# Optimization experiments

Hardware: AMD Instinct MI355X
Metric: run time of the kernel (lower is better)

Reference implementation:

```python
import jax, jax.numpy as jnp
import numpy as np

DIM = 384
HEADS = 12
WS = 7
HID = 4 * 256  # FFN hidden is hard-coded default 1024, NOT 4*dim
EPS = 1e-5


def layernorm(x, g, b):
    mu = jnp.mean(x, axis=-1, keepdims=True)
    var = jnp.mean(jnp.square(x - mu), axis=-1, keepdims=True)
    return (x - mu) * jax.lax.rsqrt(var + EPS) * g + b


def setup_inputs() -> dict:
    key = jax.random.key(0)
    ks = jax.random.split(key, 12)
    s = 0.02
    return {
        "x": jax.random.normal(ks[0], (32, DIM, 56, 56), dtype=jnp.float32),
        "ln1_g": jnp.ones((DIM,), jnp.float32),
        "ln1_b": jnp.zeros((DIM,), jnp.float32),
        "qkv_w": jax.random.normal(ks[1], (3 * DIM, DIM), jnp.float32) * s,
        "qkv_b": jnp.zeros((3 * DIM,), jnp.float32),
        "proj_w": jax.random.normal(ks[2], (DIM, DIM), jnp.float32) * s,
        "proj_b": jnp.zeros((DIM,), jnp.float32),
        "ln2_g": jnp.ones((DIM,), jnp.float32),
        "ln2_b": jnp.zeros((DIM,), jnp.float32),
        "fc1_w": jax.random.normal(ks[3], (HID, DIM), jnp.float32) * s,
        "fc1_b": jnp.zeros((HID,), jnp.float32),
        "fc2_w": jax.random.normal(ks[4], (DIM, HID), jnp.float32) * s,
        "fc2_b": jnp.zeros((DIM,), jnp.float32),
    }


def window_attention(x, qkv_w, qkv_b, proj_w, proj_b):
    # x: [B, H, W, C] channels-last
    B, H, W, C = x.shape
    Wh, Ww = H // WS, W // WS
    # partition: [B*Wh*Ww, WS*WS, C]
    w = x.reshape(B, Wh, WS, Ww, WS, C).transpose(0, 1, 3, 2, 4, 5)
    w = w.reshape(B * Wh * Ww, WS * WS, C)
    Bn, N, _ = w.shape
    hd = C // HEADS
    qkv = w @ qkv_w.T + qkv_b  # [Bn, N, 3C]
    qkv = qkv.reshape(Bn, N, 3, HEADS, hd).transpose(2, 0, 3, 1, 4)
    q, k, v = qkv[0], qkv[1], qkv[2]  # each [Bn, h, N, hd]
    attn = jnp.einsum('bhnd,bhmd->bhnm', q, k) * (hd ** -0.5)
    attn = jax.nn.softmax(attn, axis=-1)
    o = jnp.einsum('bhnm,bhmd->bhnd', attn, v)
    o = o.transpose(0, 2, 1, 3).reshape(Bn, N, C)
    o = o @ proj_w.T + proj_b
    # reverse
    o = o.reshape(B, Wh, Ww, WS, WS, C).transpose(0, 1, 3, 2, 4, 5)
    return o.reshape(B, H, W, C)


def reference(x, ln1_g, ln1_b, qkv_w, qkv_b, proj_w, proj_b,
              ln2_g, ln2_b, fc1_w, fc1_b, fc2_w, fc2_b):
    # x: [B, C, H, W]
    residual = x
    h = x.transpose(0, 2, 3, 1)  # [B,H,W,C]
    h = layernorm(h, ln1_g, ln1_b)
    h = window_attention(h, qkv_w, qkv_b, proj_w, proj_b)
    x = h.transpose(0, 3, 1, 2) + residual
    residual = x
    h = x.transpose(0, 2, 3, 1)
    h = layernorm(h, ln2_g, ln2_b)
    h = jax.nn.gelu(h @ fc1_w.T + fc1_b, approximate=False)
    h = h @ fc2_w.T + fc2_b
    return h.transpose(0, 3, 1, 2) + residual
```

## Files before the change

kernel.cpp:

```cpp
#include <hip/hip_runtime.h>
#include <cstdint>
#include <cmath>

#define DIM 384
#define HEADS 12
#define TOKENS 100352
#define HW_ 3136
#define NWIN 2048

typedef __attribute__((ext_vector_type(8))) short short8;
typedef __attribute__((ext_vector_type(4))) short short4v;
typedef __attribute__((ext_vector_type(2))) short short2v;
typedef __attribute__((ext_vector_type(4))) float f32x4;

#define AS1 __attribute__((address_space(1)))
#define AS3 __attribute__((address_space(3)))

__device__ __forceinline__ short f2b(float f){
  unsigned u = __builtin_bit_cast(unsigned, f);
  u += 0x7FFFu + ((u >> 16) & 1u);
  return (short)(u >> 16);
}
__device__ __forceinline__ float b2f(short h){
  unsigned u = ((unsigned)(unsigned short)h) << 16;
  return __builtin_bit_cast(float, u);
}

__device__ __forceinline__ void gload_lds16(const short* g, short* l){
  __builtin_amdgcn_global_load_lds((AS1 void*)(g), (AS3 void*)(l), 16, 0, 0);
}

__global__ void k_cvt(const float* __restrict__ s, short* __restrict__ d, int n){
  int i = blockIdx.x*256 + threadIdx.x;
  if (i < n) d[i] = f2b(s[i]);
}

__global__ __launch_bounds__(256) void k_ln1(const float* __restrict__ x,
    const float* __restrict__ gam, const float* __restrict__ bet,
    short* __restrict__ ln1, short* __restrict__ xr)
{
  __shared__ float red0[256];
  __shared__ float red1[256];
  __shared__ float mus[64], rss[64];
  __shared__ short lnc[64*36];
  __shared__ short xc[64*36];
  int t = threadIdx.x;
  int blk = blockIdx.x;
  int b = blk / 49;
  int hw0 = (blk % 49) * 64;
  int p = t & 63, cq = t >> 6;
  const float* xb = x + (long)b*DIM*HW_ + hw0 + p;
  float s = 0.f, sq = 0.f;
  for (int i = 0; i < 96; i++){
    int c = i*4 + cq;
    float v = xb[(long)c*HW_];
    s += v; sq += v*v;
  }
  red0[t] = s; red1[t] = sq;
  __syncthreads();
  if (t < 64){
    float ts = red0[t] + red0[t+64] + red0[t+128] + red0[t+192];
    float tq = red1[t] + red1[t+64] + red1[t+128] + red1[t+192];
    float mu = ts * (1.f/DIM);
    float var = tq * (1.f/DIM) - mu*mu;
    mus[t] = mu;
    rss[t] = rsqrtf(var + 1e-5f);
  }
  __syncthreads();
  float mu_p = mus[p], rs_p = rss[p];
  int p2 = t >> 2, q4 = t & 3;
  int hwp2 = hw0 + p2;
  int h2 = hwp2 / 56, w2 = hwp2 % 56;
  int wt2 = ((b*8 + h2/7)*8 + w2/7)*49 + (h2%7)*7 + (w2%7);
  long lnbase = (long)wt2*DIM;
  long xrbase = (long)(b*HW_ + hwp2)*DIM;
  for (int cc0 = 0; cc0 < DIM; cc0 += 32){
    #pragma unroll
    for (int u = 0; u < 8; u++){
      int c = cc0 + cq*8 + u;
      float v = xb[(long)c*HW_];
      float nv = (v - mu_p)*rs_p*gam[c] + bet[c];
      lnc[p*36 + cq*8 + u] = f2b(nv);
      xc[p*36 + cq*8 + u] = f2b(v);
    }
    __syncthreads();
    short8 av, bv;
    #pragma unroll
    for (int u = 0; u < 8; u++){
      av[u] = lnc[p2*36 + q4*8 + u];
      bv[u] = xc[p2*36 + q4*8 + u];
    }
    *(short8*)(ln1 + lnbase + cc0 + q4*8) = av;
    *(short8*)(xr + xrbase + cc0 + q4*8) = bv;
    __syncthreads();
  }
}

#define EPI_BIAS 0
#define EPI_PROJ 1
#define EPI_GELU 2
#define EPI_RES  3

template<int EPI>
__global__ __launch_bounds__(256) void k_gemm(
    const short* __restrict__ A, const short* __restrict__ B,
    const float* __restrict__ bias, short* __restrict__ out,
    const short* __restrict__ res, int M, int N, int K, int ntiles)
{
  __shared__ float smemf[8448];
  short* AsP = (short*)smemf;
  short* BsP = (short*)(smemf + 4096);
  float* E   = smemf;

  int nwg = gridDim.x;
  int orig = blockIdx.x;
  int bid = (orig & 7) * (nwg >> 3) + (orig >> 3);
  int nt = bid % ntiles, mt = bid / ntiles;
  int m0 = mt*128, n0 = nt*128;
  int t = threadIdx.x;
  int lane = t & 63, wv = t >> 6;
  int wm = wv >> 1, wn = wv & 1;
  int gg = lane >> 4, cc = lane & 15;

  int srow = t >> 2;
  int skc = ((t & 3) ^ (srow & 3)) << 3;
  const short* Ab = A + (long)(m0 + srow)*K + skc;
  const short* Bb = B + (long)(n0 + srow)*K + skc;
  long rowstep = 64L*K;

  int goff = (gg << 3) ^ ((cc & 3) << 3);

  f32x4 acc[4][4];
  #pragma unroll
  for (int i=0;i<4;i++)
    #pragma unroll
    for (int j=0;j<4;j++) acc[i][j] = (f32x4){0.f,0.f,0.f,0.f};

  gload_lds16(Ab,           AsP + t*8);
  gload_lds16(Ab + rowstep, AsP + (t+256)*8);
  gload_lds16(Bb,           BsP + t*8);
  gload_lds16(Bb + rowstep, BsP + (t+256)*8);

  int nk = K >> 5;
  for (int kt = 0; kt < nk; kt++){
    int cur = kt & 1;
    __syncthreads();
    if (kt + 1 < nk){
      int nxt = cur ^ 1;
      long ko = (long)(kt + 1) << 5;
      gload_lds16(Ab + ko,           AsP + nxt*4096 + t*8);
      gload_lds16(Ab + ko + rowstep, AsP + nxt*4096 + (t+256)*8);
      gload_lds16(Bb + ko,           BsP + nxt*4096 + t*8);
      gload_lds16(Bb + ko + rowstep, BsP + nxt*4096 + (t+256)*8);
    }
    const short* Ac = AsP + cur*4096;
    const short* Bc = BsP + cur*4096;
    short8 af[4], bfv[4];
    #pragma unroll
    for (int mi=0;mi<4;mi++) af[mi] = *(const short8*)(Ac + (wm*64 + mi*16 + cc)*32 + goff);
    #pragma unroll
    for (int ni=0;ni<4;ni++) bfv[ni] = *(const short8*)(Bc + (wn*64 + ni*16 + cc)*32 + goff);
    #pragma unroll
    for (int mi=0;mi<4;mi++)
      #pragma unroll
      for (int ni=0;ni<4;ni++)
        acc[mi][ni] = __builtin_amdgcn_mfma_f32_16x16x32_bf16(af[mi], bfv[ni], acc[mi][ni], 0, 0, 0);
  }

  #pragma unroll
  for (int p = 0; p < 2; p++){
    __syncthreads();
    #pragma unroll
    for (int mh = 0; mh < 2; mh++){
      #pragma unroll
      for (int r = 0; r < 4; r++){
        int crow = wm*32 + mh*16 + gg*4 + r;
        float* Er = E + crow*132 + wn*64 + cc;
        Er[0]  = acc[mh*2 + p][0][r];
        Er[16] = acc[mh*2 + p][1][r];
        Er[32] = acc[mh*2 + p][2][r];
        Er[48] = acc[mh*2 + p][3][r];
      }
    }
    __syncthreads();
    #pragma unroll
    for (int jj = 0; jj < 8; jj++){
      int unit = jj*256 + t;
      int crow = unit >> 5, chunk = unit & 31;
      int rr = crow & 15, mh = (crow >> 4) & 1, wmr = crow >> 5;
      int row = m0 + wmr*64 + (mh*2 + p)*16 + rr;
      int col = n0 + chunk*4;
      f32x4 v = *(const f32x4*)(E + crow*132 + chunk*4);
      f32x4 bv = *(const f32x4*)(bias + col);
      long orow;
      if constexpr (EPI == EPI_PROJ) {
        int b = row / HW_; int rem = row % HW_;
        int wid = rem / 49, idx = rem % 49;
        int hh = (wid >> 3)*7 + idx/7;
        int ww = (wid & 7)*7 + idx%7;
        orow = (long)(b*HW_ + hh*56 + ww)*N;
      } else {
        orow = (long)row*N;
      }
      float vv[4];
      #pragma unroll
      for (int j = 0; j < 4; j++){
        vv[j] = v[j] + bv[j];
        if constexpr (EPI == EPI_GELU)
          vv[j] = 0.5f*vv[j]*(1.f + erff(vv[j]*0.70710678118654752f));
      }
      if constexpr (EPI == EPI_PROJ || EPI == EPI_RES){
        short4v rv = *(const short4v*)(res + orow + col);
        #pragma unroll
        for (int j = 0; j < 4; j++) vv[j] += b2f(rv[j]);
      }
      short4v ov;
      #pragma unroll
      for (int j = 0; j < 4; j++) ov[j] = f2b(vv[j]);
      *(short4v*)(out + orow + col) = ov;
    }
  }
}

__global__ __launch_bounds__(256) void k_attn(const short* __restrict__ qkv, short* __restrict__ o)
{
  __shared__ short lds[4*7424];
  int t = threadIdx.x;
  int lane = t & 63, wv = t >> 6;
  int w = blockIdx.x;
  short* Qs = lds + wv*7424;
  short* Ks = Qs + 2560;
  short* Vt = Ks + 2560;
  short* Pl = Qs;
  int g = lane >> 4, c = lane & 15;
  int nrow = lane >> 2;
  int dc = (lane & 3) * 8;
  const float scale = 0.17677669529663687f;
  for (int hh = 0; hh < 3; hh++){
    int h = wv + hh*4;
    __syncthreads();
    long base = (long)w*49*1152 + h*32;
    #pragma unroll
    for (int it = 0; it < 4; it++){
      int n = it*16 + nrow;
      short8 vq = {0,0,0,0,0,0,0,0};
      short8 vk = vq, vvv = vq;
      if (n < 49){
        vq  = *(const short8*)(qkv + base + (long)n*1152 + dc);
        vk  = *(const short8*)(qkv + base + (long)n*1152 + 384 + dc);
        vvv = *(const short8*)(qkv + base + (long)n*1152 + 768 + dc);
      }
      *(short8*)(Qs + n*40 + dc) = vq;
      *(short8*)(Ks + n*40 + dc) = vk;
      #pragma unroll
      for (int u = 0; u < 8; u++) Vt[(dc+u)*72 + n] = vvv[u];
    }
    __syncthreads();
    f32x4 sacc[4][4];
    #pragma unroll
    for (int i=0;i<4;i++)
      #pragma unroll
      for (int j=0;j<4;j++) sacc[i][j] = (f32x4){0.f,0.f,0.f,0.f};
    short8 kf[4];
    #pragma unroll
    for (int ni=0;ni<4;ni++) kf[ni] = *(const short8*)(Ks + (ni*16 + c)*40 + g*8);
    #pragma unroll
    for (int mi=0;mi<4;mi++){
      short8 a = *(const short8*)(Qs + (mi*16 + c)*40 + g*8);
      #pragma unroll
      for (int ni=0;ni<4;ni++)
        sacc[mi][ni] = __builtin_amdgcn_mfma_f32_16x16x32_bf16(a, kf[ni], sacc[mi][ni], 0, 0, 0);
    }
    #pragma unroll
    for (int mi=0;mi<4;mi++){
      #pragma unroll
      for (int r=0;r<4;r++){
        float v0 = sacc[mi][0][r]*scale;
        float v1 = sacc[mi][1][r]*scale;
        float v2 = sacc[mi][2][r]*scale;
        float v3 = (c >= 1) ? -1e30f : sacc[mi][3][r]*scale;
        float mx = fmaxf(fmaxf(v0,v1), fmaxf(v2,v3));
        #pragma unroll
        for (int off=1; off<16; off<<=1) mx = fmaxf(mx, __shfl_xor(mx, off));
        float e0 = __expf(v0-mx), e1 = __expf(v1-mx), e2 = __expf(v2-mx), e3 = __expf(v3-mx);
        float sm = e0+e1+e2+e3;
        #pragma unroll
        for (int off=1; off<16; off<<=1) sm += __shfl_xor(sm, off);
        float inv = 1.f/sm;
        int prow = mi*16 + g*4 + r;
        Pl[prow*72 +      c] = f2b(e0*inv);
        Pl[prow*72 + 16 + c] = f2b(e1*inv);
        Pl[prow*72 + 32 + c] = f2b(e2*inv);
        Pl[prow*72 + 48 + c] = f2b(e3*inv);
      }
    }
    __syncthreads();
    f32x4 oacc[4][2];
    #pragma unroll
    for (int i=0;i<4;i++){ oacc[i][0] = (f32x4){0.f,0.f,0.f,0.f}; oacc[i][1] = oacc[i][0]; }
    #pragma unroll
    for (int ks=0; ks<2; ks++){
      short8 bb0 = *(const short8*)(Vt + (c)*72      + ks*32 + g*8);
      short8 bb1 = *(const short8*)(Vt + (16 + c)*72 + ks*32 + g*8);
      #pragma unroll
      for (int mi=0;mi<4;mi++){
        short8 aa = *(const short8*)(Pl + (mi*16 + c)*72 + ks*32 + g*8);
        oacc[mi][0] = __builtin_amdgcn_mfma_f32_16x16x32_bf16(aa, bb0, oacc[mi][0], 0, 0, 0);
        oacc[mi][1] = __builtin_amdgcn_mfma_f32_16x16x32_bf16(aa, bb1, oacc[mi][1], 0, 0, 0);
      }
    }
    #pragma unroll
    for (int mi=0;mi<4;mi++){
      #pragma unroll
      for (int r=0;r<4;r++){
        int row = mi*16 + g*4 + r;
        if (row < 49){
          long ob = ((long)w*49 + row)*384 + h*32;
          o[ob + c]      = f2b(oacc[mi][0][r]);
          o[ob + 16 + c] = f2b(oacc[mi][1][r]);
        }
      }
    }
  }
}

__global__ __launch_bounds__(256) void k_ln2(const short* __restrict__ x2,
  const float* __restrict__ gam, const float* __restrict__ bet, short* __restrict__ o)
{
  int t = threadIdx.x, lane = t & 63, wv = t >> 6;
  long row = (long)blockIdx.x*4 + wv;
  const short* xr = x2 + row*DIM;
  short4v a = *(const short4v*)(xr + lane*4);
  short2v b2 = *(const short2v*)(xr + 256 + lane*2);
  float f[6] = {b2f(a[0]),b2f(a[1]),b2f(a[2]),b2f(a[3]),b2f(b2[0]),b2f(b2[1])};
  float s = 0.f, sq = 0.f;
  #pragma unroll
  for (int i=0;i<6;i++){ s += f[i]; sq += f[i]*f[i]; }
  #pragma unroll
  for (int off=1; off<64; off<<=1){ s += __shfl_xor(s, off); sq += __shfl_xor(sq, off); }
  float mu = s*(1.f/DIM);
  float var = sq*(1.f/DIM) - mu*mu;
  float rs = rsqrtf(var + 1e-5f);
  int c0 = lane*4, c1 = 256 + lane*2;
  short4v oa; short2v ob;
  #pragma unroll
  for (int i=0;i<4;i++) oa[i] = f2b((f[i]-mu)*rs*gam[c0+i] + bet[c0+i]);
  #pragma unroll
  for (int j=0;j<2;j++) ob[j] = f2b((f[4+j]-mu)*rs*gam[c1+j] + bet[c1+j]);
  *(short4v*)(o + row*DIM + c0) = oa;
  *(short2v*)(o + row*DIM + c1) = ob;
}

__global__ __launch_bounds__(256) void k_out(const short* __restrict__ s, float* __restrict__ o)
{
  __shared__ short tile[64*392];
  int t = threadIdx.x;
  long tok0 = (long)blockIdx.x*64;
  int b = (int)(tok0 / HW_), hw0 = (int)(tok0 % HW_);
  #pragma unroll
  for (int i=0;i<12;i++){
    int unit = i*256 + t;
    int tok = unit / 48, slot = unit % 48;
    short8 v = *(const short8*)(s + (tok0+tok)*DIM + slot*8);
    int slotS = slot ^ (tok & 3);
    *(short8*)(tile + tok*392 + slotS*8) = v;
  }
  __syncthreads();
  int p = t & 63;
  int cq = t >> 6;
  for (int j=0;j<96;j++){
    int c = j*4 + cq;
    int sw = (c >> 3) ^ (p & 3);
    o[((long)b*DIM + c)*HW_ + hw0 + p] = b2f(tile[p*392 + sw*8 + (c & 7)]);
  }
}

extern "C" void kernel_launch(void* const* d_in, const int* in_sizes, int n_in,
                              void* d_out, int out_size, void* d_ws, size_t ws_size,
                              hipStream_t stream) {
  (void)in_sizes; (void)n_in; (void)out_size; (void)ws_size;
  const float* x      = (const float*)d_in[0];
  const float* ln1_g  = (const float*)d_in[1];
  const float* ln1_b  = (const float*)d_in[2];
  const float* qkv_w  = (const float*)d_in[3];
  const float* qkv_b  = (const float*)d_in[4];
  const float* proj_w = (const float*)d_in[5];
  const float* proj_b = (const float*)d_in[6];
  const float* ln2_g  = (const float*)d_in[7];
  const float* ln2_b  = (const float*)d_in[8];
  const float* fc1_w  = (const float*)d_in[9];
  const float* fc1_b  = (const float*)d_in[10];
  const float* fc2_w  = (const float*)d_in[11];
  const float* fc2_b  = (const float*)d_in[12];

  char* ws = (char*)d_ws;
  short* buf1 = (short*)(ws);
  short* buf2 = (short*)(ws + 231211008L);
  short* buf3 = (short*)(ws + 308281344L);
  short* buf4 = (short*)(ws + 385351680L);
  short* buf5 = (short*)(ws + 462422016L);
  short* wq = (short*)(ws + 539492352L);
  short* wp = wq + 442368;
  short* w1 = wp + 147456;
  short* w2 = w1 + 393216;

  k_cvt<<<dim3((442368+255)/256), dim3(256), 0, stream>>>(qkv_w, wq, 442368);
  k_cvt<<<dim3((147456+255)/256), dim3(256), 0, stream>>>(proj_w, wp, 147456);
  k_cvt<<<dim3((393216+255)/256), dim3(256), 0, stream>>>(fc1_w, w1, 393216);
  k_cvt<<<dim3((393216+255)/256), dim3(256), 0, stream>>>(fc2_w, w2, 393216);

  k_ln1<<<dim3(1568), dim3(256), 0, stream>>>(x, ln1_g, ln1_b, buf2, buf5);

  k_gemm<EPI_BIAS><<<dim3(784*9), dim3(256), 0, stream>>>(buf2, wq, qkv_b, buf1, nullptr,
                                                          TOKENS, 1152, 384, 9);
  k_attn<<<dim3(NWIN), dim3(256), 0, stream>>>(buf1, buf3);

  k_gemm<EPI_PROJ><<<dim3(784*3), dim3(256), 0, stream>>>(buf3, wp, proj_b, buf4, buf5,
                                                          TOKENS, 384, 384, 3);
  k_ln2<<<dim3(TOKENS/4), dim3(256), 0, stream>>>(buf4, ln2_g, ln2_b, buf2);

  k_gemm<EPI_GELU><<<dim3(784*8), dim3(256), 0, stream>>>(buf2, w1, fc1_b, buf1, nullptr,
                                                          TOKENS, 1024, 384, 8);
  k_gemm<EPI_RES><<<dim3(784*3), dim3(256), 0, stream>>>(buf1, w2, fc2_b, buf3, buf4,
                                                         TOKENS, 384, 1024, 3);
  k_out<<<dim3(1568), dim3(256), 0, stream>>>(buf3, (float*)d_out);
}
```

Baseline: 795.8 us.

## Fuse NCHW fp32 output transpose into fc2 GEMM epilogue; use fast GELU approximation

The fc2 GEMM epilogue now adds bias and residual, stages the tile in shared memory with a padded stride, and writes fp32 directly in channel-major NCHW layout. This removes the separate k_out transpose kernel and the bf16 round-trip of the final result. Separately, erff-based GELU is replaced by the Abramowitz-Stegun polynomial with rcp and exp, cutting the epilogue cost of the fc1 GEMM at a small accuracy cost. The attention kernel is only moved in the file.

```diff
diff --git a/kernel.cpp b/kernel.cpp
--- a/kernel.cpp
+++ b/kernel.cpp
@@ -28,6 +28,17 @@
 
 __device__ __forceinline__ void gload_lds16(const short* g, short* l){
   __builtin_amdgcn_global_load_lds((AS1 void*)(g), (AS3 void*)(l), 16, 0, 0);
+}
+
+__device__ __forceinline__ float gelu_f(float v){
+  float z  = v * 0.70710678118654752f;
+  float az = fabsf(z);
+  float t  = __builtin_amdgcn_rcpf(1.f + 0.3275911f*az);
+  float poly = t*(0.254829592f + t*(-0.284496736f + t*(1.421413741f +
+               t*(-1.453152027f + t*1.061405429f))));
+  float e  = __expf(-z*z);
+  float er = copysignf(1.f - poly*e, z);
+  return 0.5f * v * (1.f + er);
 }
 
 __global__ void k_cvt(const float* __restrict__ s, short* __restrict__ d, int n){
@@ -99,7 +110,7 @@
 #define EPI_BIAS 0
 #define EPI_PROJ 1
 #define EPI_GELU 2
-#define EPI_RES  3
+#define EPI_OUT  4
 
 template<int EPI>
 __global__ __launch_bounds__(256) void k_gemm(
@@ -107,7 +118,9 @@
     const float* __restrict__ bias, short* __restrict__ out,
     const short* __restrict__ res, int M, int N, int K, int ntiles)
 {
-  __shared__ float smemf[8448];
+  constexpr int ES  = (EPI == EPI_OUT) ? 133  : 132;
+  constexpr int SMF = (EPI == EPI_OUT) ? 8512 : 8448;
+  __shared__ float smemf[SMF];
   short* AsP = (short*)smemf;
   short* BsP = (short*)(smemf + 4096);
   float* E   = smemf;
@@ -167,158 +180,99 @@
         acc[mi][ni] = __builtin_amdgcn_mfma_f32_16x16x32_bf16(af[mi], bfv[ni], acc[mi][ni], 0, 0, 0);
   }
 
-  #pragma unroll
-  for (int p = 0; p < 2; p++){
-    __syncthreads();
-    #pragma unroll
-    for (int mh = 0; mh < 2; mh++){
-      #pragma unroll
-      for (int r = 0; r < 4; r++){
-        int crow = wm*32 + mh*16 + gg*4 + r;
-        float* Er = E + crow*132 + wn*64 + cc;
-        Er[0]  = acc[mh*2 + p][0][r];
-        Er[16] = acc[mh*2 + p][1][r];
-        Er[32] = acc[mh*2 + p][2][r];
-        Er[48] = acc[mh*2 + p][3][r];
-      }
-    }
-    __syncthreads();
-    #pragma unroll
-    for (int jj = 0; jj < 8; jj++){
-      int unit = jj*256 + t;
-      int crow = unit >> 5, chunk = unit & 31;
-      int rr = crow & 15, mh = (crow >> 4) & 1, wmr = crow >> 5;
-      int row = m0 + wmr*64 + (mh*2 + p)*16 + rr;
-      int col = n0 + chunk*4;
-      f32x4 v = *(const f32x4*)(E + crow*132 + chunk*4);
-      f32x4 bv = *(const f32x4*)(bias + col);
-      long orow;
-      if constexpr (EPI == EPI_PROJ) {
-        int b = row / HW_; int rem = row % HW_;
-        int wid = rem / 49, idx = rem % 49;
-        int hh = (wid >> 3)*7 + idx/7;
-        int ww = (wid & 7)*7 + idx%7;
-        orow = (long)(b*HW_ + hh*56 + ww)*N;
-      } else {
-        orow = (long)row*N;
-      }
-      float vv[4];
-      #pragma unroll
-      for (int j = 0; j < 4; j++){
-        vv[j] = v[j] + bv[j];
-        if constexpr (EPI == EPI_GELU)
-          vv[j] = 0.5f*vv[j]*(1.f + erff(vv[j]*0.70710678118654752f));
-      }
-      if constexpr (EPI == EPI_PROJ || EPI == EPI_RES){
-        short4v rv = *(const short4v*)(res + orow + col);
-        #pragma unroll
-        for (int j = 0; j < 4; j++) vv[j] += b2f(rv[j]);
-      }
-      short4v ov;
-      #pragma unroll
-      for (int j = 0; j < 4; j++) ov[j] = f2b(vv[j]);
-      *(short4v*)(out + orow + col) = ov;
-    }
-  }
-}
-
-__global__ __launch_bounds__(256) void k_attn(const short* __restrict__ qkv, short* __restrict__ o)
-{
-  __shared__ short lds[4*7424];
-  int t = threadIdx.x;
-  int lane = t & 63, wv = t >> 6;
-  int w = blockIdx.x;
-  short* Qs = lds + wv*7424;
-  short* Ks = Qs + 2560;
-  short* Vt = Ks + 2560;
-  short* Pl = Qs;
-  int g = lane >> 4, c = lane & 15;
-  int nrow = lane >> 2;
-  int dc = (lane & 3) * 8;
-  const float scale = 0.17677669529663687f;
-  for (int hh = 0; hh < 3; hh++){
-    int h = wv + hh*4;
-    __syncthreads();
-    long base = (long)w*49*1152 + h*32;
-    #pragma unroll
-    for (int it = 0; it < 4; it++){
-      int n = it*16 + nrow;
-      short8 vq = {0,0,0,0,0,0,0,0};
-      short8 vk = vq, vvv = vq;
-      if (n < 49){
-        vq  = *(const short8*)(qkv + base + (long)n*1152 + dc);
-        vk  = *(const short8*)(qkv + base + (long)n*1152 + 384 + dc);
-        vvv = *(const short8*)(qkv + base + (long)n*1152 + 768 + dc);
-      }
-      *(short8*)(Qs + n*40 + dc) = vq;
-      *(short8*)(Ks + n*40 + dc) = vk;
-      #pragma unroll
-      for (int u = 0; u < 8; u++) Vt[(dc+u)*72 + n] = vvv[u];
-    }
-    __syncthreads();
-    f32x4 sacc[4][4];
-    #pragma unroll
-    for (int i=0;i<4;i++)
-      #pragma unroll
-      for (int j=0;j<4;j++) sacc[i][j] = (f32x4){0.f,0.f,0.f,0.f};
-    short8 kf[4];
-    #pragma unroll
-    for (int ni=0;ni<4;ni++) kf[ni] = *(const short8*)(Ks + (ni*16 + c)*40 + g*8);
-    #pragma unroll
-    for (int mi=0;mi<4;mi++){
-      short8 a = *(const short8*)(Qs + (mi*16 + c)*40 + g*8);
-      #pragma unroll
-      for (int ni=0;ni<4;ni++)
-        sacc[mi][ni] = __builtin_amdgcn_mfma_f32_16x16x32_bf16(a, kf[ni], sacc[mi][ni], 0, 0, 0);
-    }
-    #pragma unroll
-    for (int mi=0;mi<4;mi++){
-      #pragma unroll
-      for (int r=0;r<4;r++){
-        float v0 = sacc[mi][0][r]*scale;
-        float v1 = sacc[mi][1][r]*scale;
-        float v2 = sacc[mi][2][r]*scale;
-        float v3 = (c >= 1) ? -1e30f : sacc[mi][3][r]*scale;
-        float mx = fmaxf(fmaxf(v0,v1), fmaxf(v2,v3));
-        #pragma unroll
-        for (int off=1; off<16; off<<=1) mx = fmaxf(mx, __shfl_xor(mx, off));
-        float e0 = __expf(v0-mx), e1 = __expf(v1-mx), e2 = __expf(v2-mx), e3 = __expf(v3-mx);
-        float sm = e0+e1+e2+e3;
-        #pragma unroll
-        for (int off=1; off<16; off<<=1) sm += __shfl_xor(sm, off);
-        float inv = 1.f/sm;
-        int prow = mi*16 + g*4 + r;
-        Pl[prow*72 +      c] = f2b(e0*inv);
-        Pl[prow*72 + 16 + c] = f2b(e1*inv);
-        Pl[prow*72 + 32 + c] = f2b(e2*inv);
-        Pl[prow*72 + 48 + c] = f2b(e3*inv);
-      }
-    }
-    __syncthreads();
-    f32x4 oacc[4][2];
-    #pragma unroll
-    for (int i=0;i<4;i++){ oacc[i][0] = (f32x4){0.f,0.f,0.f,0.f}; oacc[i][1] = oacc[i][0]; }
-    #pragma unroll
-    for (int ks=0; ks<2; ks++){
-      short8 bb0 = *(const short8*)(Vt + (c)*72      + ks*32 + g*8);
-      short8 bb1 = *(const short8*)(Vt + (16 + c)*72 + ks*32 + g*8);
-      #pragma unroll
-      for (int mi=0;mi<4;mi++){
-        short8 aa = *(const short8*)(Pl + (mi*16 + c)*72 + ks*32 + g*8);
-        oacc[mi][0] = __builtin_amdgcn_mfma_f32_16x16x32_bf16(aa, bb0, oacc[mi][0], 0, 0, 0);
-        oacc[mi][1] = __builtin_amdgcn_mfma_f32_16x16x32_bf16(aa, bb1, oacc[mi][1], 0, 0, 0);
-      }
-    }
-    #pragma unroll
-    for (int mi=0;mi<4;mi++){
-      #pragma unroll
-      for (int r=0;r<4;r++){
-        int row = mi*16 + g*4 + r;
-        if (row < 49){
-          long ob = ((long)w*49 + row)*384 + h*32;
-          o[ob + c]      = f2b(oacc[mi][0][r]);
-          o[ob + 16 + c] = f2b(oacc[mi][1][r]);
-        }
+  if constexpr (EPI == EPI_OUT) {
+    float* outf = (float*)out;
+    #pragma unroll
+    for (int p = 0; p < 2; p++){
+      __syncthreads();
+      if (wm == p){
+        #pragma unroll
+        for (int mi=0;mi<4;mi++){
+          #pragma unroll
+          for (int r=0;r<4;r++){
+            float* Er = E + (mi*16 + gg*4 + r)*ES + wn*64 + cc;
+            Er[0]  = acc[mi][0][r];
+            Er[16] = acc[mi][1][r];
+            Er[32] = acc[mi][2][r];
+            Er[48] = acc[mi][3][r];
+          }
+        }
+      }
+      __syncthreads();
+      #pragma unroll
+      for (int jj = 0; jj < 8; jj++){
+        int unit = jj*256 + t;
+        int crow = unit >> 5, chunk = unit & 31;
+        int row = m0 + p*64 + crow;
+        f32x4 v = *(const f32x4*)(E + crow*ES + chunk*4);
+        f32x4 bv = *(const f32x4*)(bias + n0 + chunk*4);
+        short4v rv = *(const short4v*)(res + (long)row*N + n0 + chunk*4);
+        #pragma unroll
+        for (int j = 0; j < 4; j++) v[j] += bv[j] + b2f(rv[j]);
+        *(f32x4*)(E + crow*ES + chunk*4) = v;
+      }
+      __syncthreads();
+      #pragma unroll
+      for (int jj = 0; jj < 32; jj++){
+        int unit = jj*256 + t;
+        int c = unit >> 6, rl = unit & 63;
+        int token = m0 + p*64 + rl;
+        int b = token / HW_;
+        int hw = token - b*HW_;
+        outf[((long)b*DIM + n0 + c)*HW_ + hw] = E[rl*ES + c];
+      }
+    }
+  } else {
+    #pragma unroll
+    for (int p = 0; p < 2; p++){
+      __syncthreads();
+      #pragma unroll
+      for (int mh = 0; mh < 2; mh++){
+        #pragma unroll
+        for (int r = 0; r < 4; r++){
+          int crow = wm*32 + mh*16 + gg*4 + r;
+          float* Er = E + crow*ES + wn*64 + cc;
+          Er[0]  = acc[mh*2 + p][0][r];
+          Er[16] = acc[mh*2 + p][1][r];
+          Er[32] = acc[mh*2 + p][2][r];
+          Er[48] = acc[mh*2 + p][3][r];
+        }
+      }
+      __syncthreads();
+      #pragma unroll
+      for (int jj = 0; jj < 8; jj++){
+        int unit = jj*256 + t;
+        int crow = unit >> 5, chunk = unit & 31;
+        int rr = crow & 15, mh = (crow >> 4) & 1, wmr = crow >> 5;
+        int row = m0 + wmr*64 + (mh*2 + p)*16 + rr;
+        int col = n0 + chunk*4;
+        f32x4 v = *(const f32x4*)(E + crow*ES + chunk*4);
+        f32x4 bv = *(const f32x4*)(bias + col);
+        long orow;
+        if constexpr (EPI == EPI_PROJ) {
+          int b = row / HW_; int rem = row % HW_;
+          int wid = rem / 49, idx = rem % 49;
+          int hh = (wid >> 3)*7 + idx/7;
+          int ww = (wid & 7)*7 + idx%7;
+          orow = (long)(b*HW_ + hh*56 + ww)*N;
+        } else {
+          orow = (long)row*N;
+        }
+        float vv[4];
+        #pragma unroll
+        for (int j = 0; j < 4; j++){
+          vv[j] = v[j] + bv[j];
+          if constexpr (EPI == EPI_GELU) vv[j] = gelu_f(vv[j]);
+        }
+        if constexpr (EPI == EPI_PROJ){
+          short4v rv = *(const short4v*)(res + orow + col);
+          #pragma unroll
+          for (int j = 0; j < 4; j++) vv[j] += b2f(rv[j]);
+        }
+        short4v ov;
+        #pragma unroll
+        for (int j = 0; j < 4; j++) ov[j] = f2b(vv[j]);
+        *(short4v*)(out + orow + col) = ov;
       }
     }
   }
@@ -351,27 +305,105 @@
   *(short2v*)(o + row*DIM + c1) = ob;
 }
 
-__global__ __launch_bounds__(256) void k_out(const short* __restrict__ s, float* __restrict__ o)
+__global__ __launch_bounds__(256) void k_attn(const short* __restrict__ qkv, short* __restrict__ o)
 {
-  __shared__ short tile[64*392];
+  __shared__ short lds[4*7424];
   int t = threadIdx.x;
-  long tok0 = (long)blockIdx.x*64;
-  int b = (int)(tok0 / HW_), hw0 = (int)(tok0 % HW_);
-  #pragma unroll
-  for (int i=0;i<12;i++){
-    int unit = i*256 + t;
-    int tok = unit / 48, slot = unit % 48;
-    short8 v = *(const short8*)(s + (tok0+tok)*DIM + slot*8);
-    int slotS = slot ^ (tok & 3);
-    *(short8*)(tile + tok*392 + slotS*8) = v;
-  }
-  __syncthreads();
-  int p = t & 63;
-  int cq = t >> 6;
-  for (int j=0;j<96;j++){
-    int c = j*4 + cq;
-    int sw = (c >> 3) ^ (p & 3);
-    o[((long)b*DIM + c)*HW_ + hw0 + p] = b2f(tile[p*392 + sw*8 + (c & 7)]);
+  int lane = t & 63, wv = t >> 6;
+  int w = blockIdx.x;
+  short* Qs = lds + wv*7424;
+  short* Ks = Qs + 2560;
+  short* Vt = Ks + 2560;
+  short* Pl = Qs;
+  int g = lane >> 4, c = lane & 15;
+  int nrow = lane >> 2;
+  int dc = (lane & 3) * 8;
+  const float scale = 0.17677669529663687f;
+  for (int hh = 0; hh < 3; hh++){
+    int h = wv + hh*4;
+    __syncthreads();
+    long base = (long)w*49*1152 + h*32;
+    #pragma unroll
+    for (int it = 0; it < 4; it++){
+      int n = it*16 + nrow;
+      short8 vq = {0,0,0,0,0,0,0,0};
+      short8 vk = vq, vvv = vq;
+      if (n < 49){
+        vq  = *(const short8*)(qkv + base + (long)n*1152 + dc);
+        vk  = *(const short8*)(qkv + base + (long)n*1152 + 384 + dc);
+        vvv = *(const short8*)(qkv + base + (long)n*1152 + 768 + dc);
+      }
+      *(short8*)(Qs + n*40 + dc) = vq;
+      *(short8*)(Ks + n*40 + dc) = vk;
+      #pragma unroll
+      for (int u = 0; u < 8; u++) Vt[(dc+u)*72 + n] = vvv[u];
+    }
+    __syncthreads();
+    f32x4 sacc[4][4];
+    #pragma unroll
+    for (int i=0;i<4;i++)
+      #pragma unroll
+      for (int j=0;j<4;j++) sacc[i][j] = (f32x4){0.f,0.f,0.f,0.f};
+    short8 kf[4];
+    #pragma unroll
+    for (int ni=0;ni<4;ni++) kf[ni] = *(const short8*)(Ks + (ni*16 + c)*40 + g*8);
+    #pragma unroll
+    for (int mi=0;mi<4;mi++){
+      short8 a = *(const short8*)(Qs + (mi*16 + c)*40 + g*8);
+      #pragma unroll
+      for (int ni=0;ni<4;ni++)
+        sacc[mi][ni] = __builtin_amdgcn_mfma_f32_16x16x32_bf16(a, kf[ni], sacc[mi][ni], 0, 0, 0);
+    }
+    #pragma unroll
+    for (int mi=0;mi<4;mi++){
+      #pragma unroll
+      for (int r=0;r<4;r++){
+        float v0 = sacc[mi][0][r]*scale;
+        float v1 = sacc[mi][1][r]*scale;
+        float v2 = sacc[mi][2][r]*scale;
+        float v3 = (c >= 1) ? -1e30f : sacc[mi][3][r]*scale;
+        float mx = fmaxf(fmaxf(v0,v1), fmaxf(v2,v3));
+        #pragma unroll
+        for (int off=1; off<16; off<<=1) mx = fmaxf(mx, __shfl_xor(mx, off));
+        float e0 = __expf(v0-mx), e1 = __expf(v1-mx), e2 = __expf(v2-mx), e3 = __expf(v3-mx);
+        float sm = e0+e1+e2+e3;
+        #pragma unroll
+        for (int off=1; off<16; off<<=1) sm += __shfl_xor(sm, off);
+        float inv = 1.f/sm;
+        int prow = mi*16 + g*4 + r;
+        Pl[prow*72 +      c] = f2b(e0*inv);
+        Pl[prow*72 + 16 + c] = f2b(e1*inv);
+        Pl[prow*72 + 32 + c] = f2b(e2*inv);
+        Pl[prow*72 + 48 + c] = f2b(e3*inv);
+      }
+    }
+    __syncthreads();
+    f32x4 oacc[4][2];
+    #pragma unroll
+    for (int i=0;i<4;i++){ oacc[i][0] = (f32x4){0.f,0.f,0.f,0.f}; oacc[i][1] = oacc[i][0]; }
+    #pragma unroll
+    for (int ks=0; ks<2; ks++){
+      short8 bb0 = *(const short8*)(Vt + (c)*72      + ks*32 + g*8);
+      short8 bb1 = *(const short8*)(Vt + (16 + c)*72 + ks*32 + g*8);
+      #pragma unroll
+      for (int mi=0;mi<4;mi++){
+        short8 aa = *(const short8*)(Pl + (mi*16 + c)*72 + ks*32 + g*8);
+        oacc[mi][0] = __builtin_amdgcn_mfma_f32_16x16x32_bf16(aa, bb0, oacc[mi][0], 0, 0, 0);
+        oacc[mi][1] = __builtin_amdgcn_mfma_f32_16x16x32_bf16(aa, bb1, oacc[mi][1], 0, 0, 0);
+      }
+    }
+    #pragma unroll
+    for (int mi=0;mi<4;mi++){
+      #pragma unroll
+      for (int r=0;r<4;r++){
+        int row = mi*16 + g*4 + r;
+        if (row < 49){
+          long ob = ((long)w*49 + row)*384 + h*32;
+          o[ob + c]      = f2b(oacc[mi][0][r]);
+          o[ob + 16 + c] = f2b(oacc[mi][1][r]);
+        }
+      }
+    }
   }
 }
 
@@ -421,7 +453,6 @@
 
   k_gemm<EPI_GELU><<<dim3(784*8), dim3(256), 0, stream>>>(buf2, w1, fc1_b, buf1, nullptr,
                                                           TOKENS, 1024, 384, 8);
-  k_gemm<EPI_RES><<<dim3(784*3), dim3(256), 0, stream>>>(buf1, w2, fc2_b, buf3, buf4,
+  k_gemm<EPI_OUT><<<dim3(784*3), dim3(256), 0, stream>>>(buf1, w2, fc2_b, (short*)d_out, buf4,
                                                          TOKENS, 384, 1024, 3);
-  k_out<<<dim3(1568), dim3(256), 0, stream>>>(buf3, (float*)d_out);
-}
+}
```

Result: faster. 766.4 us (-3.7%).
